# Kernel optimization log

Hardware: AMD Instinct MI355X
Metric: run time of the kernel (lower is better)

## Reference

```python
import jax, jax.numpy as jnp
import numpy as np

N, K, P_DIM, HID, NCLS = 20000, 16, 63, 32 + 0, 32
HID = 128
IN_DIM = P_DIM + 1


def setup_inputs() -> dict:
    key = jax.random.key(0)
    ks = iter(jax.random.split(key, 64))

    def nrm(shape, s=0.1):
        return jax.random.normal(next(ks), shape, jnp.float32) * s

    inp = {
        "p": nrm((N, P_DIM), 1.0),
        "neigh_idx": jax.random.randint(next(ks), (N, K), 0, N, dtype=jnp.int32),
    }
    dims = [(IN_DIM, HID), (HID, HID), (HID, NCLS)]
    for l, (din, dout) in enumerate(dims):
        inp[f"l{l}_Wih"] = nrm((4 * din, din))
        inp[f"l{l}_Whh"] = nrm((4 * din, din))
        inp[f"l{l}_bih"] = jnp.zeros((4 * din,), jnp.float32)
        inp[f"l{l}_bhh"] = jnp.zeros((4 * din,), jnp.float32)
        inp[f"l{l}_Wself"] = nrm((dout, din))
        inp[f"l{l}_Wneigh"] = nrm((dout, din))
        inp[f"l{l}_b"] = jnp.zeros((dout,), jnp.float32)
    return inp


def _lstm_agg(feat, neigh_idx, Wih, Whh, bih, bhh):
    # Per-node LSTM over the K in-neighbor features (DGL _lstm_reducer).
    n, h_dim = feat.shape[0], Whh.shape[1]
    bias = bih + bhh

    def step(carry, idx_t):
        h, c = carry
        x = feat[idx_t]                                   # [N, Din] gather (step t message)
        g = x @ Wih.T + h @ Whh.T + bias                  # [N, 4H]
        i, f, gg, o = jnp.split(g, 4, axis=-1)            # torch LSTM gate order i,f,g,o
        c = jax.nn.sigmoid(f) * c + jax.nn.sigmoid(i) * jnp.tanh(gg)
        h = jax.nn.sigmoid(o) * jnp.tanh(c)
        return (h, c), None

    init = (jnp.zeros((n, h_dim), feat.dtype), jnp.zeros((n, h_dim), feat.dtype))
    (h, _), _ = jax.lax.scan(step, init, neigh_idx.T)     # scan over K neighbor slots
    return h                                              # final hidden state = neigh feat


def _forward(p, neigh_idx, *params):
    # features = cat(in_degree/N, p); fixed-degree graph -> in_degree == K
    deg = jnp.full((p.shape[0], 1), K / N, p.dtype)
    feat = jnp.concatenate([deg, p], axis=1)
    layers = [params[7 * l: 7 * (l + 1)] for l in range(3)]
    for l, (Wih, Whh, bih, bhh, Wself, Wneigh, b) in enumerate(layers):
        neigh = _lstm_agg(feat, neigh_idx, Wih, Whh, bih, bhh)
        feat = feat @ Wself.T + neigh @ Wneigh.T + b      # fc_self + fc_neigh + bias
        if l < 2:
            feat = jax.nn.relu(feat)
    return feat


def reference(p, neigh_idx,
              l0_Wih, l0_Whh, l0_bih, l0_bhh, l0_Wself, l0_Wneigh, l0_b,
              l1_Wih, l1_Whh, l1_bih, l1_bhh, l1_Wself, l1_Wneigh, l1_b,
              l2_Wih, l2_Whh, l2_bih, l2_bhh, l2_Wself, l2_Wneigh, l2_b):
    return _forward(p, neigh_idx,
                    l0_Wih, l0_Whh, l0_bih, l0_bhh, l0_Wself, l0_Wneigh, l0_b,
                    l1_Wih, l1_Whh, l1_bih, l1_bhh, l1_Wself, l1_Wneigh, l1_b,
                    l2_Wih, l2_Whh, l2_bih, l2_bhh, l2_Wself, l2_Wneigh, l2_b)
```

## Files before the change

kernel.cpp:

```cpp
#include <hip/hip_runtime.h>
#include <hip/hip_bf16.h>
#include <stdint.h>


#define N_NODES 20000
#define KNE 16

typedef __bf16 bf16x8 __attribute__((ext_vector_type(8)));
typedef float f32x4 __attribute__((ext_vector_type(4)));

__device__ __forceinline__ bf16x8 ldb8(const __hip_bfloat16* p) {
  uint4 u = *reinterpret_cast<const uint4*>(p);
  return __builtin_bit_cast(bf16x8, u);
}
__device__ __forceinline__ void pin(bf16x8& v) {
  uint4 u = __builtin_bit_cast(uint4, v);
  asm volatile("" : "+v"(u.x), "+v"(u.y), "+v"(u.z), "+v"(u.w));
  v = __builtin_bit_cast(bf16x8, u);
}
__device__ __forceinline__ float b2f_lo(uint32_t u) {
  return __builtin_bit_cast(float, u << 16);
}
__device__ __forceinline__ float b2f_hi(uint32_t u) {
  return __builtin_bit_cast(float, u & 0xffff0000u);
}
__device__ __forceinline__ uint32_t pk2(float a, float b) {
  uint32_t ua = (uint32_t)__builtin_bit_cast(unsigned short, __float2bfloat16(a));
  uint32_t ub = (uint32_t)__builtin_bit_cast(unsigned short, __float2bfloat16(b));
  return ua | (ub << 16);
}
__device__ __forceinline__ float sigf(float x) {
  float t = __builtin_amdgcn_exp2f(-1.442695041f * x);
  return __builtin_amdgcn_rcpf(1.f + t);
}
__device__ __forceinline__ float tanhf_(float x) {
  float t = __builtin_amdgcn_exp2f(2.885390082f * x);
  return 1.f - 2.f * __builtin_amdgcn_rcpf(t + 1.f);
}

__global__ void build_feat0(const float* __restrict__ p,
                            __hip_bfloat16* __restrict__ f0) {
  int i = blockIdx.x * 256 + threadIdx.x;
  if (i >= N_NODES * 64) return;
  int n = i >> 6, c = i & 63;
  float v = (c == 0) ? ((float)KNE / (float)N_NODES) : p[n * 63 + c - 1];
  f0[i] = __float2bfloat16(v);
}

struct CvtArgs {
  const float* s[12];
  __hip_bfloat16* d[12];
  int off[13];
};
__global__ void cvt_all(CvtArgs a) {
  int i = blockIdx.x * 256 + threadIdx.x;
  if (i >= a.off[12]) return;
#pragma unroll
  for (int k = 0; k < 12; ++k)
    if (i >= a.off[k] && i < a.off[k + 1]) {
      int j = i - a.off[k];
      a.d[k][j] = __float2bfloat16(a.s[k][j]);
    }
}

template <int DIN, int DOUT>
__global__ __launch_bounds__(256, 2) void proj_kern(
    const __hip_bfloat16* __restrict__ feat,
    const __hip_bfloat16* __restrict__ Wih,
    const float* __restrict__ bih,
    const float* __restrict__ bhh,
    const __hip_bfloat16* __restrict__ Wself,
    const float* __restrict__ bvec,
    __hip_bfloat16* __restrict__ P, float* __restrict__ S) {
  constexpr int KB = DIN / 32;
  constexpr int CCT = DIN / 16;
  constexpr int CTS = DOUT / 16;
  const int n0 = blockIdx.x * 32;
  const int tid = threadIdx.x;
  const int wv = tid >> 6;
  const int lane = tid & 63;
  const int quad = lane >> 4;
  const int c16 = lane & 15;

  bf16x8 afr[2][KB];
#pragma unroll
  for (int rt = 0; rt < 2; ++rt)
#pragma unroll
    for (int kb = 0; kb < KB; ++kb)
      afr[rt][kb] =
          ldb8(feat + (size_t)(n0 + rt * 16 + c16) * DIN + kb * 32 + quad * 8);

  const f32x4 zz = {0.f, 0.f, 0.f, 0.f};
  for (int ct = wv; ct < CCT + CTS; ct += 4) {
    if (ct < CCT) {
      const int cc = ct * 16 + c16;
      f32x4 ag[4][2];
#pragma unroll
      for (int g = 0; g < 4; ++g) { ag[g][0] = zz; ag[g][1] = zz; }
#pragma unroll
      for (int kb = 0; kb < KB; ++kb)
#pragma unroll
        for (int g = 0; g < 4; ++g) {
          bf16x8 b = ldb8(Wih + (size_t)(g * DIN + cc) * DIN + kb * 32 +
                          quad * 8);
          ag[g][0] = __builtin_amdgcn_mfma_f32_16x16x32_bf16(afr[0][kb], b,
                                                             ag[g][0], 0, 0, 0);
          ag[g][1] = __builtin_amdgcn_mfma_f32_16x16x32_bf16(afr[1][kb], b,
                                                             ag[g][1], 0, 0, 0);
        }
      float bi = bih[cc] + bhh[cc];
      float bff = bih[DIN + cc] + bhh[DIN + cc];
      float bg = bih[2 * DIN + cc] + bhh[2 * DIN + cc];
      float bo = bih[3 * DIN + cc] + bhh[3 * DIN + cc];
      uint2* Pp = reinterpret_cast<uint2*>(P);
#pragma unroll
      for (int rt = 0; rt < 2; ++rt)
#pragma unroll
        for (int r = 0; r < 4; ++r) {
          int n = n0 + rt * 16 + quad * 4 + r;
          uint2 u;
          u.x = pk2(ag[0][rt][r] + bi, ag[1][rt][r] + bff);
          u.y = pk2(ag[2][rt][r] + bg, ag[3][rt][r] + bo);
          Pp[(size_t)n * DIN + cc] = u;
        }
    } else {
      const int c = (ct - CCT) * 16 + c16;
      f32x4 a0 = zz, a1 = zz;
#pragma unroll
      for (int kb = 0; kb < KB; ++kb) {
        bf16x8 b = ldb8(Wself + (size_t)c * DIN + kb * 32 + quad * 8);
        a0 = __builtin_amdgcn_mfma_f32_16x16x32_bf16(afr[0][kb], b, a0, 0, 0, 0);
        a1 = __builtin_amdgcn_mfma_f32_16x16x32_bf16(afr[1][kb], b, a1, 0, 0, 0);
      }
      float bias = bvec[c];
#pragma unroll
      for (int r = 0; r < 4; ++r) {
        S[(size_t)(n0 + quad * 4 + r) * DOUT + c] = a0[r] + bias;
        S[(size_t)(n0 + 16 + quad * 4 + r) * DOUT + c] = a1[r] + bias;
      }
    }
  }
}

template <int DIN, int DOUT, int NT, bool RELU, typename OutT>
__global__ __launch_bounds__((DIN / 16) * 64)
__attribute__((amdgpu_waves_per_eu(4))) void lstm_fc_kern(
    const __hip_bfloat16* __restrict__ P,
    const float* __restrict__ S,
    const __hip_bfloat16* __restrict__ Whh,
    const __hip_bfloat16* __restrict__ Wng,
    const int* __restrict__ nidx,
    OutT* __restrict__ outp) {
  constexpr int W = DIN / 16;
  constexpr int KB = DIN / 32;
  constexpr int HS = DIN + 8;
  constexpr int NN = 16 * NT;

  __shared__ __align__(16) __hip_bfloat16 hl[2][NN * HS];
  __shared__ int idxl[NN * KNE];

  const int n0 = blockIdx.x * NN;
  const int tid = threadIdx.x;
  const int wv = tid >> 6;
  const int lane = tid & 63;
  const int quad = lane >> 4;
  const int c16 = lane & 15;
  const int col = wv * 16 + c16;

  for (int i = tid; i < NN * KNE; i += W * 64) idxl[i] = nidx[n0 * KNE + i];
  __syncthreads();

  uint2 pf[2][NT][4];
  auto loadpf = [&](int t, int b) {
#pragma unroll
    for (int nt = 0; nt < NT; ++nt)
#pragma unroll
      for (int r = 0; r < 4; ++r) {
        int src = idxl[(nt * 16 + quad * 4 + r) * KNE + t];
        pf[b][nt][r] =
            reinterpret_cast<const uint2*>(P + (size_t)src * (4 * DIN))[col];
      }
  };

  loadpf(0, 0);

  bf16x8 Bp[4][KB];
#pragma unroll
  for (int g = 0; g < 4; ++g)
#pragma unroll
    for (int kb = 0; kb < KB; ++kb) {
      Bp[g][kb] =
          ldb8(Whh + (size_t)(g * DIN + col) * DIN + kb * 32 + quad * 8);
      pin(Bp[g][kb]);
    }

  loadpf(1, 1);

  float cst[NT][4];
#pragma unroll
  for (int nt = 0; nt < NT; ++nt)
#pragma unroll
    for (int r = 0; r < 4; ++r) cst[nt][r] = 0.f;

  auto initag = [&](int b, int nt, f32x4 (&ag)[4]) {
#pragma unroll
    for (int r = 0; r < 4; ++r) {
      ag[0][r] = b2f_lo(pf[b][nt][r].x);
      ag[1][r] = b2f_hi(pf[b][nt][r].x);
      ag[2][r] = b2f_lo(pf[b][nt][r].y);
      ag[3][r] = b2f_hi(pf[b][nt][r].y);
    }
  };

  auto gates = [&](int hb, int nt, const f32x4 (&ag)[4]) {
#pragma unroll
    for (int r = 0; r < 4; ++r) {
      float cc =
          sigf(ag[1][r]) * cst[nt][r] + sigf(ag[0][r]) * tanhf_(ag[2][r]);
      cst[nt][r] = cc;
      hl[hb][(nt * 16 + quad * 4 + r) * HS + col] =
          __float2bfloat16(sigf(ag[3][r]) * tanhf_(cc));
    }
  };

#pragma unroll
  for (int nt = 0; nt < NT; ++nt) {
    f32x4 ag[4];
    initag(0, nt, ag);
    gates(0, nt, ag);
  }

#pragma unroll
  for (int t = 1; t < KNE; ++t) {
    __syncthreads();
    if (t + 1 < KNE) loadpf(t + 1, (t + 1) & 1);
    const int pb = (t - 1) & 1;
#pragma unroll
    for (int nt = 0; nt < NT; ++nt) {
      bf16x8 Af[KB];
#pragma unroll
      for (int kb = 0; kb < KB; ++kb)
        Af[kb] = ldb8(&hl[pb][(nt * 16 + c16) * HS + kb * 32 + quad * 8]);
      f32x4 ag[4];
      initag(t & 1, nt, ag);
#pragma unroll
      for (int kb = 0; kb < KB; ++kb)
#pragma unroll
        for (int g = 0; g < 4; ++g)
          ag[g] = __builtin_amdgcn_mfma_f32_16x16x32_bf16(Af[kb], Bp[g][kb],
                                                          ag[g], 0, 0, 0);
      gates(t & 1, nt, ag);
    }
  }

  const f32x4 zz = {0.f, 0.f, 0.f, 0.f};
  __syncthreads();
  bf16x8 Hf[NT][KB];
#pragma unroll
  for (int nt = 0; nt < NT; ++nt)
#pragma unroll
    for (int kb = 0; kb < KB; ++kb)
      Hf[nt][kb] = ldb8(&hl[1][(nt * 16 + c16) * HS + kb * 32 + quad * 8]);
  for (int ct = wv; ct < DOUT / 16; ct += W) {
    f32x4 a[NT];
#pragma unroll
    for (int nt = 0; nt < NT; ++nt) a[nt] = zz;
#pragma unroll
    for (int kb = 0; kb < KB; ++kb) {
      bf16x8 b = ldb8(Wng + (size_t)(ct * 16 + c16) * DIN + kb * 32 + quad * 8);
#pragma unroll
      for (int nt = 0; nt < NT; ++nt)
        a[nt] = __builtin_amdgcn_mfma_f32_16x16x32_bf16(Hf[nt][kb], b, a[nt],
                                                        0, 0, 0);
    }
#pragma unroll
    for (int nt = 0; nt < NT; ++nt)
#pragma unroll
      for (int r = 0; r < 4; ++r) {
        int n = n0 + nt * 16 + quad * 4 + r;
        int c = ct * 16 + c16;
        float v = a[nt][r] + S[(size_t)n * DOUT + c];
        if (RELU) v = fmaxf(v, 0.f);
        if constexpr (sizeof(OutT) == 2)
          outp[(size_t)n * DOUT + c] = __float2bfloat16(v);
        else
          outp[(size_t)n * DOUT + c] = v;
      }
  }
}

extern "C" void kernel_launch(void* const* d_in, const int* in_sizes, int n_in,
                              void* d_out, int out_size, void* d_ws,
                              size_t ws_size, hipStream_t stream) {
  (void)in_sizes; (void)n_in; (void)out_size; (void)ws_size;
  const float* p = (const float*)d_in[0];
  const int* nidx = (const int*)d_in[1];
  const float* L[3][7];
  for (int l = 0; l < 3; ++l)
    for (int j = 0; j < 7; ++j)
      L[l][j] = (const float*)d_in[2 + 7 * l + j];

  char* w = (char*)d_ws;
  __hip_bfloat16* feat0 = (__hip_bfloat16*)(w);
  __hip_bfloat16* feat1 = (__hip_bfloat16*)(w + 2560000);
  __hip_bfloat16* feat2 = (__hip_bfloat16*)(w + 7680000);
  __hip_bfloat16* Pb    = (__hip_bfloat16*)(w + 12800000);
  float*          Sb    = (float*)(w + 33280000);
  __hip_bfloat16* wb    = (__hip_bfloat16*)(w + 43520000);

  const int din_[3] = {64, 128, 128}, dout_[3] = {128, 128, 32};
  __hip_bfloat16 *Wih_b[3], *Whh_b[3], *Wself_b[3], *Wng_b[3];
  CvtArgs ca;
  size_t off = 0;
  int k = 0, pre = 0;
  for (int l = 0; l < 3; ++l) {
    int din = din_[l], dout = dout_[l];
    int n0 = 4 * din * din, n2 = dout * din;
    Wih_b[l] = wb + off;   off += (size_t)n0;
    Whh_b[l] = wb + off;   off += (size_t)n0;
    Wself_b[l] = wb + off; off += (size_t)n2;
    Wng_b[l] = wb + off;   off += (size_t)n2;
    const float* srcs[4] = {L[l][0], L[l][1], L[l][4], L[l][5]};
    __hip_bfloat16* dsts[4] = {Wih_b[l], Whh_b[l], Wself_b[l], Wng_b[l]};
    int ns[4] = {n0, n0, n2, n2};
    for (int j = 0; j < 4; ++j) {
      ca.s[k] = srcs[j];
      ca.d[k] = dsts[j];
      ca.off[k] = pre;
      pre += ns[j];
      ++k;
    }
  }
  ca.off[12] = pre;

  cvt_all<<<(pre + 255) / 256, 256, 0, stream>>>(ca);
  build_feat0<<<(N_NODES * 64 + 255) / 256, 256, 0, stream>>>(p, feat0);

  proj_kern<64, 128><<<N_NODES / 32, 256, 0, stream>>>(
      feat0, Wih_b[0], L[0][2], L[0][3], Wself_b[0], L[0][6], Pb, Sb);
  lstm_fc_kern<64, 128, 2, true, __hip_bfloat16>
      <<<N_NODES / 32, 256, 0, stream>>>(Pb, Sb, Whh_b[0], Wng_b[0], nidx,
                                         feat1);

  proj_kern<128, 128><<<N_NODES / 32, 256, 0, stream>>>(
      feat1, Wih_b[1], L[1][2], L[1][3], Wself_b[1], L[1][6], Pb, Sb);
  lstm_fc_kern<128, 128, 1, true, __hip_bfloat16>
      <<<N_NODES / 16, 512, 0, stream>>>(Pb, Sb, Whh_b[1], Wng_b[1], nidx,
                                         feat2);

  proj_kern<128, 32><<<N_NODES / 32, 256, 0, stream>>>(
      feat2, Wih_b[2], L[2][2], L[2][3], Wself_b[2], L[2][6], Pb, Sb);
  lstm_fc_kern<128, 32, 1, false, float>
      <<<N_NODES / 16, 512, 0, stream>>>(Pb, Sb, Whh_b[2], Wng_b[2], nidx,
                                         (float*)d_out);
}
```

Before: 347.2 us.

## Fuse feature build and next-layer projection into LSTM kernels, prescale gate weights

Moves feature construction into the first projection kernel and runs the next layer's input projection inside each LSTM+fc kernel from shared memory, so the intermediate feature tensors no longer go through global memory and three launches disappear. Gate weights and biases are prescaled by -log2(e) or 2·log2(e) at conversion time, so the sigmoid and tanh evaluations skip one multiply each. A dedicated final-layer kernel writes the fp32 output. The fused kernels use more shared memory and registers, which may reduce occupancy.

```diff
diff --git a/kernel.cpp b/kernel.cpp
--- a/kernel.cpp
+++ b/kernel.cpp
@@ -5,6 +5,8 @@
 
 #define N_NODES 20000
 #define KNE 16
+#define C1F 1.442695041f
+#define C2F 2.885390082f
 
 typedef __bf16 bf16x8 __attribute__((ext_vector_type(8)));
 typedef float f32x4 __attribute__((ext_vector_type(4)));
@@ -29,28 +31,12 @@
   uint32_t ub = (uint32_t)__builtin_bit_cast(unsigned short, __float2bfloat16(b));
   return ua | (ub << 16);
 }
-__device__ __forceinline__ float sigf(float x) {
-  float t = __builtin_amdgcn_exp2f(-1.442695041f * x);
-  return __builtin_amdgcn_rcpf(1.f + t);
-}
-__device__ __forceinline__ float tanhf_(float x) {
-  float t = __builtin_amdgcn_exp2f(2.885390082f * x);
-  return 1.f - 2.f * __builtin_amdgcn_rcpf(t + 1.f);
-}
-
-__global__ void build_feat0(const float* __restrict__ p,
-                            __hip_bfloat16* __restrict__ f0) {
-  int i = blockIdx.x * 256 + threadIdx.x;
-  if (i >= N_NODES * 64) return;
-  int n = i >> 6, c = i & 63;
-  float v = (c == 0) ? ((float)KNE / (float)N_NODES) : p[n * 63 + c - 1];
-  f0[i] = __float2bfloat16(v);
-}
 
 struct CvtArgs {
   const float* s[12];
   __hip_bfloat16* d[12];
   int off[13];
+  int gsz[12];
 };
 __global__ void cvt_all(CvtArgs a) {
   int i = blockIdx.x * 256 + threadIdx.x;
@@ -59,22 +45,102 @@
   for (int k = 0; k < 12; ++k)
     if (i >= a.off[k] && i < a.off[k + 1]) {
       int j = i - a.off[k];
-      a.d[k][j] = __float2bfloat16(a.s[k][j]);
-    }
-}
-
-template <int DIN, int DOUT>
-__global__ __launch_bounds__(256, 2) void proj_kern(
-    const __hip_bfloat16* __restrict__ feat,
+      float v = a.s[k][j];
+      if (a.gsz[k]) {
+        int g = j / a.gsz[k];
+        v *= (g == 2) ? C2F : -C1F;
+      }
+      a.d[k][j] = __float2bfloat16(v);
+    }
+}
+
+template <int DIN, int DOUT, int NTR, int WW>
+__device__ __forceinline__ void proj_phase(
+    const __hip_bfloat16* sA,
     const __hip_bfloat16* __restrict__ Wih,
-    const float* __restrict__ bih,
-    const float* __restrict__ bhh,
+    const float* __restrict__ bih, const float* __restrict__ bhh,
+    const __hip_bfloat16* __restrict__ Wself,
+    const float* __restrict__ bvec,
+    __hip_bfloat16* __restrict__ P, float* __restrict__ S,
+    int n0, int wv, int quad, int c16) {
+  constexpr int KB = DIN / 32;
+  constexpr int CCT = DIN / 16;
+  constexpr int CTS = DOUT / 16;
+  constexpr int HS = DIN + 8;
+  const f32x4 zz = {0.f, 0.f, 0.f, 0.f};
+  bf16x8 afr[NTR][KB];
+#pragma unroll
+  for (int nt = 0; nt < NTR; ++nt)
+#pragma unroll
+    for (int kb = 0; kb < KB; ++kb)
+      afr[nt][kb] = ldb8(&sA[(nt * 16 + c16) * HS + kb * 32 + quad * 8]);
+
+  for (int ct = wv; ct < CCT + CTS; ct += WW) {
+    if (ct < CCT) {
+      const int cc = ct * 16 + c16;
+      f32x4 ag[4][NTR];
+#pragma unroll
+      for (int g = 0; g < 4; ++g)
+#pragma unroll
+        for (int nt = 0; nt < NTR; ++nt) ag[g][nt] = zz;
+#pragma unroll
+      for (int kb = 0; kb < KB; ++kb)
+#pragma unroll
+        for (int g = 0; g < 4; ++g) {
+          bf16x8 b =
+              ldb8(Wih + (size_t)(g * DIN + cc) * DIN + kb * 32 + quad * 8);
+#pragma unroll
+          for (int nt = 0; nt < NTR; ++nt)
+            ag[g][nt] = __builtin_amdgcn_mfma_f32_16x16x32_bf16(
+                afr[nt][kb], b, ag[g][nt], 0, 0, 0);
+        }
+      float bi = -C1F * (bih[cc] + bhh[cc]);
+      float bf_ = -C1F * (bih[DIN + cc] + bhh[DIN + cc]);
+      float bg = C2F * (bih[2 * DIN + cc] + bhh[2 * DIN + cc]);
+      float bo = -C1F * (bih[3 * DIN + cc] + bhh[3 * DIN + cc]);
+      uint2* Pp = reinterpret_cast<uint2*>(P);
+#pragma unroll
+      for (int nt = 0; nt < NTR; ++nt)
+#pragma unroll
+        for (int r = 0; r < 4; ++r) {
+          int n = n0 + nt * 16 + quad * 4 + r;
+          uint2 u;
+          u.x = pk2(ag[0][nt][r] + bi, ag[1][nt][r] + bf_);
+          u.y = pk2(ag[2][nt][r] + bg, ag[3][nt][r] + bo);
+          Pp[(size_t)n * DIN + cc] = u;
+        }
+    } else {
+      const int c = (ct - CCT) * 16 + c16;
+      f32x4 a[NTR];
+#pragma unroll
+      for (int nt = 0; nt < NTR; ++nt) a[nt] = zz;
+#pragma unroll
+      for (int kb = 0; kb < KB; ++kb) {
+        bf16x8 b = ldb8(Wself + (size_t)c * DIN + kb * 32 + quad * 8);
+#pragma unroll
+        for (int nt = 0; nt < NTR; ++nt)
+          a[nt] = __builtin_amdgcn_mfma_f32_16x16x32_bf16(afr[nt][kb], b,
+                                                          a[nt], 0, 0, 0);
+      }
+      float bias = bvec[c];
+#pragma unroll
+      for (int nt = 0; nt < NTR; ++nt)
+#pragma unroll
+        for (int r = 0; r < 4; ++r)
+          S[(size_t)(n0 + nt * 16 + quad * 4 + r) * DOUT + c] =
+              a[nt][r] + bias;
+    }
+  }
+}
+
+__global__ __launch_bounds__(256, 2) void feat_proj0(
+    const float* __restrict__ p,
+    const __hip_bfloat16* __restrict__ Wih,
+    const float* __restrict__ bih, const float* __restrict__ bhh,
     const __hip_bfloat16* __restrict__ Wself,
     const float* __restrict__ bvec,
     __hip_bfloat16* __restrict__ P, float* __restrict__ S) {
-  constexpr int KB = DIN / 32;
-  constexpr int CCT = DIN / 16;
-  constexpr int CTS = DOUT / 16;
+  __shared__ __align__(16) __hip_bfloat16 sFeat[32 * 72];
   const int n0 = blockIdx.x * 32;
   const int tid = threadIdx.x;
   const int wv = tid >> 6;
@@ -82,81 +148,38 @@
   const int quad = lane >> 4;
   const int c16 = lane & 15;
 
-  bf16x8 afr[2][KB];
-#pragma unroll
-  for (int rt = 0; rt < 2; ++rt)
-#pragma unroll
-    for (int kb = 0; kb < KB; ++kb)
-      afr[rt][kb] =
-          ldb8(feat + (size_t)(n0 + rt * 16 + c16) * DIN + kb * 32 + quad * 8);
-
-  const f32x4 zz = {0.f, 0.f, 0.f, 0.f};
-  for (int ct = wv; ct < CCT + CTS; ct += 4) {
-    if (ct < CCT) {
-      const int cc = ct * 16 + c16;
-      f32x4 ag[4][2];
-#pragma unroll
-      for (int g = 0; g < 4; ++g) { ag[g][0] = zz; ag[g][1] = zz; }
-#pragma unroll
-      for (int kb = 0; kb < KB; ++kb)
-#pragma unroll
-        for (int g = 0; g < 4; ++g) {
-          bf16x8 b = ldb8(Wih + (size_t)(g * DIN + cc) * DIN + kb * 32 +
-                          quad * 8);
-          ag[g][0] = __builtin_amdgcn_mfma_f32_16x16x32_bf16(afr[0][kb], b,
-                                                             ag[g][0], 0, 0, 0);
-          ag[g][1] = __builtin_amdgcn_mfma_f32_16x16x32_bf16(afr[1][kb], b,
-                                                             ag[g][1], 0, 0, 0);
-        }
-      float bi = bih[cc] + bhh[cc];
-      float bff = bih[DIN + cc] + bhh[DIN + cc];
-      float bg = bih[2 * DIN + cc] + bhh[2 * DIN + cc];
-      float bo = bih[3 * DIN + cc] + bhh[3 * DIN + cc];
-      uint2* Pp = reinterpret_cast<uint2*>(P);
-#pragma unroll
-      for (int rt = 0; rt < 2; ++rt)
-#pragma unroll
-        for (int r = 0; r < 4; ++r) {
-          int n = n0 + rt * 16 + quad * 4 + r;
-          uint2 u;
-          u.x = pk2(ag[0][rt][r] + bi, ag[1][rt][r] + bff);
-          u.y = pk2(ag[2][rt][r] + bg, ag[3][rt][r] + bo);
-          Pp[(size_t)n * DIN + cc] = u;
-        }
-    } else {
-      const int c = (ct - CCT) * 16 + c16;
-      f32x4 a0 = zz, a1 = zz;
-#pragma unroll
-      for (int kb = 0; kb < KB; ++kb) {
-        bf16x8 b = ldb8(Wself + (size_t)c * DIN + kb * 32 + quad * 8);
-        a0 = __builtin_amdgcn_mfma_f32_16x16x32_bf16(afr[0][kb], b, a0, 0, 0, 0);
-        a1 = __builtin_amdgcn_mfma_f32_16x16x32_bf16(afr[1][kb], b, a1, 0, 0, 0);
-      }
-      float bias = bvec[c];
-#pragma unroll
-      for (int r = 0; r < 4; ++r) {
-        S[(size_t)(n0 + quad * 4 + r) * DOUT + c] = a0[r] + bias;
-        S[(size_t)(n0 + 16 + quad * 4 + r) * DOUT + c] = a1[r] + bias;
-      }
-    }
-  }
-}
-
-template <int DIN, int DOUT, int NT, bool RELU, typename OutT>
+  for (int i = tid; i < 32 * 64; i += 256) {
+    int n = i >> 6, c = i & 63;
+    float v = (c == 0) ? ((float)KNE / (float)N_NODES)
+                       : p[(size_t)(n0 + n) * 63 + c - 1];
+    sFeat[n * 72 + c] = __float2bfloat16(v);
+  }
+  __syncthreads();
+  proj_phase<64, 128, 2, 4>(sFeat, Wih, bih, bhh, Wself, bvec, P, S, n0, wv,
+                            quad, c16);
+}
+
+template <int DIN, int DOUT, int DOUTN, int NT, bool RELU>
 __global__ __launch_bounds__((DIN / 16) * 64)
-__attribute__((amdgpu_waves_per_eu(4))) void lstm_fc_kern(
+__attribute__((amdgpu_waves_per_eu(4))) void lstm_proj_kern(
     const __hip_bfloat16* __restrict__ P,
     const float* __restrict__ S,
     const __hip_bfloat16* __restrict__ Whh,
     const __hip_bfloat16* __restrict__ Wng,
     const int* __restrict__ nidx,
-    OutT* __restrict__ outp) {
+    const __hip_bfloat16* __restrict__ Wih2,
+    const float* __restrict__ bih2, const float* __restrict__ bhh2,
+    const __hip_bfloat16* __restrict__ Wself2,
+    const float* __restrict__ bvec2,
+    __hip_bfloat16* __restrict__ P2, float* __restrict__ S2) {
   constexpr int W = DIN / 16;
   constexpr int KB = DIN / 32;
   constexpr int HS = DIN + 8;
   constexpr int NN = 16 * NT;
+  constexpr int HS2 = DOUT + 8;
 
   __shared__ __align__(16) __hip_bfloat16 hl[2][NN * HS];
+  __shared__ __align__(16) __hip_bfloat16 sOut[NN * HS2];
   __shared__ int idxl[NN * KNE];
 
   const int n0 = blockIdx.x * NN;
@@ -215,11 +238,18 @@
   auto gates = [&](int hb, int nt, const f32x4 (&ag)[4]) {
 #pragma unroll
     for (int r = 0; r < 4; ++r) {
-      float cc =
-          sigf(ag[1][r]) * cst[nt][r] + sigf(ag[0][r]) * tanhf_(ag[2][r]);
+      float wi = __builtin_amdgcn_rcpf(1.f + __builtin_amdgcn_exp2f(ag[0][r]));
+      float wf = __builtin_amdgcn_rcpf(1.f + __builtin_amdgcn_exp2f(ag[1][r]));
+      float wg = __builtin_amdgcn_rcpf(1.f + __builtin_amdgcn_exp2f(ag[2][r]));
+      float wo = __builtin_amdgcn_rcpf(1.f + __builtin_amdgcn_exp2f(ag[3][r]));
+      float tg = fmaf(-2.f, wg, 1.f);
+      float cc = wf * cst[nt][r] + wi * tg;
       cst[nt][r] = cc;
+      float tc = fmaf(
+          -2.f,
+          __builtin_amdgcn_rcpf(1.f + __builtin_amdgcn_exp2f(C2F * cc)), 1.f);
       hl[hb][(nt * 16 + quad * 4 + r) * HS + col] =
-          __float2bfloat16(sigf(ag[3][r]) * tanhf_(cc));
+          __float2bfloat16(wo * tc);
     }
   };
 
@@ -281,11 +311,135 @@
         int c = ct * 16 + c16;
         float v = a[nt][r] + S[(size_t)n * DOUT + c];
         if (RELU) v = fmaxf(v, 0.f);
-        if constexpr (sizeof(OutT) == 2)
-          outp[(size_t)n * DOUT + c] = __float2bfloat16(v);
-        else
-          outp[(size_t)n * DOUT + c] = v;
+        sOut[(nt * 16 + quad * 4 + r) * HS2 + c] = __float2bfloat16(v);
       }
+  }
+  __syncthreads();
+  proj_phase<DOUT, DOUTN, NT, W>(sOut, Wih2, bih2, bhh2, Wself2, bvec2, P2,
+                                 S2, n0, wv, quad, c16);
+}
+
+template <int DIN, int DOUT>
+__global__ __launch_bounds__((DIN / 16) * 64)
+__attribute__((amdgpu_waves_per_eu(4))) void lstm_out_kern(
+    const __hip_bfloat16* __restrict__ P, const float* __restrict__ S,
+    const __hip_bfloat16* __restrict__ Whh,
+    const __hip_bfloat16* __restrict__ Wng, const int* __restrict__ nidx,
+    float* __restrict__ outp) {
+  constexpr int W = DIN / 16;
+  constexpr int KB = DIN / 32;
+  constexpr int HS = DIN + 8;
+
+  __shared__ __align__(16) __hip_bfloat16 hl[2][16 * HS];
+  __shared__ int idxl[16 * KNE];
+
+  const int n0 = blockIdx.x * 16;
+  const int tid = threadIdx.x;
+  const int wv = tid >> 6;
+  const int lane = tid & 63;
+  const int quad = lane >> 4;
+  const int c16 = lane & 15;
+  const int col = wv * 16 + c16;
+
+  for (int i = tid; i < 16 * KNE; i += W * 64) idxl[i] = nidx[n0 * KNE + i];
+  __syncthreads();
+
+  uint2 pf[2][4];
+  auto loadpf = [&](int t, int b) {
+#pragma unroll
+    for (int r = 0; r < 4; ++r) {
+      int src = idxl[(quad * 4 + r) * KNE + t];
+      pf[b][r] =
+          reinterpret_cast<const uint2*>(P + (size_t)src * (4 * DIN))[col];
+    }
+  };
+
+  loadpf(0, 0);
+  bf16x8 Bp[4][KB];
+#pragma unroll
+  for (int g = 0; g < 4; ++g)
+#pragma unroll
+    for (int kb = 0; kb < KB; ++kb) {
+      Bp[g][kb] =
+          ldb8(Whh + (size_t)(g * DIN + col) * DIN + kb * 32 + quad * 8);
+      pin(Bp[g][kb]);
+    }
+  loadpf(1, 1);
+
+  float cst[4];
+#pragma unroll
+  for (int r = 0; r < 4; ++r) cst[r] = 0.f;
+
+  auto initag = [&](int b, f32x4 (&ag)[4]) {
+#pragma unroll
+    for (int r = 0; r < 4; ++r) {
+      ag[0][r] = b2f_lo(pf[b][r].x);
+      ag[1][r] = b2f_hi(pf[b][r].x);
+      ag[2][r] = b2f_lo(pf[b][r].y);
+      ag[3][r] = b2f_hi(pf[b][r].y);
+    }
+  };
+  auto gates = [&](int hb, const f32x4 (&ag)[4]) {
+#pragma unroll
+    for (int r = 0; r < 4; ++r) {
+      float wi = __builtin_amdgcn_rcpf(1.f + __builtin_amdgcn_exp2f(ag[0][r]));
+      float wf = __builtin_amdgcn_rcpf(1.f + __builtin_amdgcn_exp2f(ag[1][r]));
+      float wg = __builtin_amdgcn_rcpf(1.f + __builtin_amdgcn_exp2f(ag[2][r]));
+      float wo = __builtin_amdgcn_rcpf(1.f + __builtin_amdgcn_exp2f(ag[3][r]));
+      float tg = fmaf(-2.f, wg, 1.f);
+      float cc = wf * cst[r] + wi * tg;
+      cst[r] = cc;
+      float tc = fmaf(
+          -2.f,
+          __builtin_amdgcn_rcpf(1.f + __builtin_amdgcn_exp2f(C2F * cc)), 1.f);
+      hl[hb][(quad * 4 + r) * HS + col] = __float2bfloat16(wo * tc);
+    }
+  };
+
+  {
+    f32x4 ag[4];
+    initag(0, ag);
+    gates(0, ag);
+  }
+#pragma unroll
+  for (int t = 1; t < KNE; ++t) {
+    __syncthreads();
+    if (t + 1 < KNE) loadpf(t + 1, (t + 1) & 1);
+    const int pb = (t - 1) & 1;
+    bf16x8 Af[KB];
+#pragma unroll
+    for (int kb = 0; kb < KB; ++kb)
+      Af[kb] = ldb8(&hl[pb][c16 * HS + kb * 32 + quad * 8]);
+    f32x4 ag[4];
+    initag(t & 1, ag);
+#pragma unroll
+    for (int kb = 0; kb < KB; ++kb)
+#pragma unroll
+      for (int g = 0; g < 4; ++g)
+        ag[g] = __builtin_amdgcn_mfma_f32_16x16x32_bf16(Af[kb], Bp[g][kb],
+                                                        ag[g], 0, 0, 0);
+    gates(t & 1, ag);
+  }
+
+  const f32x4 zz = {0.f, 0.f, 0.f, 0.f};
+  __syncthreads();
+  bf16x8 Hf[KB];
+#pragma unroll
+  for (int kb = 0; kb < KB; ++kb)
+    Hf[kb] = ldb8(&hl[1][c16 * HS + kb * 32 + quad * 8]);
+  for (int ct = wv; ct < DOUT / 16; ct += W) {
+    f32x4 a = zz;
+#pragma unroll
+    for (int kb = 0; kb < KB; ++kb) {
+      bf16x8 b = ldb8(Wng + (size_t)(ct * 16 + c16) * DIN + kb * 32 + quad * 8);
+      a = __builtin_amdgcn_mfma_f32_16x16x32_bf16(Hf[kb], b, a, 0, 0, 0);
+    }
+#pragma unroll
+    for (int r = 0; r < 4; ++r) {
+      int n = n0 + quad * 4 + r;
+      int c = ct * 16 + c16;
+      outp[(size_t)n * DOUT + c] = a[r] + S[(size_t)n * DOUT + c];
+    }
   }
 }
 
@@ -301,12 +455,13 @@
       L[l][j] = (const float*)d_in[2 + 7 * l + j];
 
   char* w = (char*)d_ws;
-  __hip_bfloat16* feat0 = (__hip_bfloat16*)(w);
-  __hip_bfloat16* feat1 = (__hip_bfloat16*)(w + 2560000);
-  __hip_bfloat16* feat2 = (__hip_bfloat16*)(w + 7680000);
-  __hip_bfloat16* Pb    = (__hip_bfloat16*)(w + 12800000);
-  float*          Sb    = (float*)(w + 33280000);
-  __hip_bfloat16* wb    = (__hip_bfloat16*)(w + 43520000);
+  __hip_bfloat16* P0 = (__hip_bfloat16*)(w);
+  float*          S0 = (float*)(w + 10240000);
+  __hip_bfloat16* P1 = (__hip_bfloat16*)(w + 20480000);
+  float*          S1 = (float*)(w + 40960000);
+  float*          S2 = (float*)(w + 51200000);
+  __hip_bfloat16* P2 = (__hip_bfloat16*)(w);
+  __hip_bfloat16* wb = (__hip_bfloat16*)(w + 53760000);
 
   const int din_[3] = {64, 128, 128}, dout_[3] = {128, 128, 32};
   __hip_bfloat16 *Wih_b[3], *Whh_b[3], *Wself_b[3], *Wng_b[3];
@@ -323,10 +478,12 @@
     const float* srcs[4] = {L[l][0], L[l][1], L[l][4], L[l][5]};
     __hip_bfloat16* dsts[4] = {Wih_b[l], Whh_b[l], Wself_b[l], Wng_b[l]};
     int ns[4] = {n0, n0, n2, n2};
+    int gs[4] = {din * din, din * din, 0, 0};
     for (int j = 0; j < 4; ++j) {
       ca.s[k] = srcs[j];
       ca.d[k] = dsts[j];
       ca.off[k] = pre;
+      ca.gsz[k] = gs[j];
       pre += ns[j];
       ++k;
     }
@@ -334,23 +491,18 @@
   ca.off[12] = pre;
 
   cvt_all<<<(pre + 255) / 256, 256, 0, stream>>>(ca);
-  build_feat0<<<(N_NODES * 64 + 255) / 256, 256, 0, stream>>>(p, feat0);
-
-  proj_kern<64, 128><<<N_NODES / 32, 256, 0, stream>>>(
-      feat0, Wih_b[0], L[0][2], L[0][3], Wself_b[0], L[0][6], Pb, Sb);
-  lstm_fc_kern<64, 128, 2, true, __hip_bfloat16>
-      <<<N_NODES / 32, 256, 0, stream>>>(Pb, Sb, Whh_b[0], Wng_b[0], nidx,
-                                         feat1);
-
-  proj_kern<128, 128><<<N_NODES / 32, 256, 0, stream>>>(
-      feat1, Wih_b[1], L[1][2], L[1][3], Wself_b[1], L[1][6], Pb, Sb);
-  lstm_fc_kern<128, 128, 1, true, __hip_bfloat16>
-      <<<N_NODES / 16, 512, 0, stream>>>(Pb, Sb, Whh_b[1], Wng_b[1], nidx,
-                                         feat2);
-
-  proj_kern<128, 32><<<N_NODES / 32, 256, 0, stream>>>(
-      feat2, Wih_b[2], L[2][2], L[2][3], Wself_b[2], L[2][6], Pb, Sb);
-  lstm_fc_kern<128, 32, 1, false, float>
-      <<<N_NODES / 16, 512, 0, stream>>>(Pb, Sb, Whh_b[2], Wng_b[2], nidx,
-                                         (float*)d_out);
-}
+
+  feat_proj0<<<N_NODES / 32, 256, 0, stream>>>(
+      p, Wih_b[0], L[0][2], L[0][3], Wself_b[0], L[0][6], P0, S0);
+
+  lstm_proj_kern<64, 128, 128, 2, true><<<N_NODES / 32, 256, 0, stream>>>(
+      P0, S0, Whh_b[0], Wng_b[0], nidx, Wih_b[1], L[1][2], L[1][3],
+      Wself_b[1], L[1][6], P1, S1);
+
+  lstm_proj_kern<128, 128, 32, 1, true><<<N_NODES / 16, 512, 0, stream>>>(
+      P1, S1, Whh_b[1], Wng_b[1], nidx, Wih_b[2], L[2][2], L[2][3],
+      Wself_b[2], L[2][6], P2, S2);
+
+  lstm_out_kern<128, 32><<<N_NODES / 16, 512, 0, stream>>>(
+      P2, S2, Whh_b[2], Wng_b[2], nidx, (float*)d_out);
+}
```

New measurement: 327.3 us (median of 2 runs). 1.06x faster.
